# Kernel optimization log

Measured on AMD Instinct MI355X. Metric: run time of the kernel, lower is better.

Reference implementation:

```python
import jax, jax.numpy as jnp
import numpy as np

D_MODEL, N_HEAD, N_BR = 768, 12, 4
DH = D_MODEL // N_HEAD            # 64
H_TOT = N_BR * N_HEAD             # 48
K_RETR = 12
MLP_SCALE = np.pi / np.sqrt(3.0)


def rmsnorm(x):
    eps = jnp.finfo(x.dtype).eps
    return x * jax.lax.rsqrt(jnp.mean(x * x, axis=-1, keepdims=True) + eps)


def setup_inputs() -> dict:
    key = jax.random.key(0)
    ks = jax.random.split(key, 16)
    B, T, C = 2, 1024, D_MODEL
    s = 0.02
    return {
        "A": jax.random.normal(ks[0], (B, T, C), jnp.float32),
        "X": jax.random.normal(ks[1], (B, T, C), jnp.float32),
        "Wq_w": jax.random.normal(ks[2], (4 * C, C), jnp.float32) * s,
        "Wq_b": jax.random.normal(ks[3], (4 * C,), jnp.float32) * s,
        "Wk_w": jax.random.normal(ks[4], (C, C), jnp.float32) * s,
        "Wk_b": jax.random.normal(ks[5], (C,), jnp.float32) * s,
        "wedge_A": jax.random.normal(ks[6], (DH, DH), jnp.float32) * s,
        "wedge_bias": jax.random.normal(ks[7], (H_TOT, DH), jnp.float32) * s,
        "sink_scalars": jax.random.normal(ks[8], (H_TOT, 1, 1), jnp.float32) * s,
        "v_nulls": jax.random.normal(ks[9], (N_BR, C), jnp.float32) * s,
        "fc_w": jax.random.normal(ks[10], (4 * DH, DH), jnp.float32) * s,
        "fc_b": jax.random.normal(ks[11], (4 * DH,), jnp.float32) * s,
        "proj_w": jax.random.normal(ks[12], (DH, 4 * DH), jnp.float32) * s,
        "proj_b": jax.random.normal(ks[13], (DH,), jnp.float32) * s,
        "WO": jax.random.normal(ks[14], (N_BR, C, C), jnp.float32) * s,
        "WO_b": jax.random.normal(ks[15], (N_BR, C), jnp.float32) * s,
    }


def reference(A, X, Wq_w, Wq_b, Wk_w, Wk_b, wedge_A, wedge_bias,
              sink_scalars, v_nulls, fc_w, fc_b, proj_w, proj_b, WO, WO_b):
    B, T, C = A.shape
    K = min(K_RETR, T)
    scale = DH ** -0.5

    # Q / K projections -> (B, H, T, Dh)
    q = (A @ Wq_w.T + Wq_b).reshape(B, T, H_TOT, DH).transpose(0, 2, 1, 3)
    q = rmsnorm(q)
    kb = (X @ Wk_w.T + Wk_b).reshape(B, T, N_HEAD, DH).transpose(0, 2, 1, 3)
    k = jnp.tile(kb, (1, N_BR, 1, 1))          # repeat sub-heads over branches
    k_vanilla = k                               # pre-wedge/pre-rope keys

    # BiasedWedge: x + x @ (skew(A) + diag(id_bias)) per head
    S = (wedge_A - wedge_A.T) + jax.vmap(jnp.diag)(wedge_bias)   # (H, Dh, Dh)
    q = q + jnp.einsum('bhtd,hde->bhte', q, S)
    k = k + jnp.einsum('bhtd,hde->bhte', k, S)

    # RoPE (interleaved halves concatenated)
    inv_freq = 1.0 / (10000.0 ** (jnp.arange(0, DH, 2, dtype=jnp.float32) / DH))
    freqs = jnp.arange(T, dtype=jnp.float32)[:, None] * inv_freq[None, :]  # (T, Dh/2)
    cos, sin = jnp.cos(freqs), jnp.sin(freqs)

    def rope(x):
        x1, x2 = x[..., 0::2], x[..., 1::2]
        return jnp.concatenate([x1 * cos - x2 * sin, x1 * sin + x2 * cos], axis=-1)

    q, k = rope(q), rope(k)

    # full causal attention with sink token
    scores = jnp.einsum('bhtd,bhsd->bhts', q, k) * scale        # (B,H,T,T)
    causal = jnp.triu(jnp.ones((T, T), bool), 1)
    scores = jnp.where(causal, -jnp.inf, scores)
    sinks = jnp.broadcast_to(sink_scalars.reshape(1, H_TOT, 1, 1), (B, H_TOT, T, 1))
    probs = jax.nn.softmax(jnp.concatenate([scores, sinks], axis=-1), axis=-1)
    probs_tok = jnp.where(causal, 0.0, probs[..., :T])
    probs_sink = probs[..., T:]                                  # (B,H,T,1)

    # top-k retrieval + gather of vanilla keys
    w, idx = jax.lax.top_k(probs_tok, K)                         # (B,H,T,K)
    bi = jnp.arange(B)[:, None, None, None]
    hi = jnp.arange(H_TOT)[None, :, None, None]
    k_sel = k_vanilla[bi, hi, idx]                               # (B,H,T,K,Dh)
    # weighted mean marker (sum is permutation-invariant, so sort is elided)
    marker = (jnp.einsum('bhtk,bhtkd->bhtd', w, k_sel) + k_vanilla) / (K + 1)

    # per-token V_net MLP on head_dim
    h = marker @ fc_w.T + fc_b
    h = h * h + 0.75 * h * h * h
    h = rmsnorm(h)
    h = h * jax.nn.sigmoid(MLP_SCALE * h)
    out_tokens = h @ proj_w.T + proj_b                           # (B,H,T,Dh)

    context = out_tokens + probs_sink * v_nulls.reshape(H_TOT, DH)[None, :, None, :]
    context = context.reshape(B, N_BR, N_HEAD, T, DH).transpose(0, 1, 3, 2, 4)
    context = context.reshape(B, N_BR, T, C)

    y = jnp.einsum('bntc,ncd->bntd', context, WO) + WO_b[None, :, None, :]
    return y.mean(axis=1)
```

## Files before the change

kernel.cpp:

```cpp
#include <hip/hip_runtime.h>
#include <math.h>

#define B_   2
#define T_   1024
#define C_   768
#define DH_  64
#define NH_  12
#define HT_  48

typedef short bf16x8 __attribute__((ext_vector_type(8)));
typedef float f32x4 __attribute__((ext_vector_type(4)));

__device__ __forceinline__ float wave_sum(float v) {
#pragma unroll
    for (int off = 32; off; off >>= 1) v += __shfl_xor(v, off, 64);
    return v;
}
__device__ __forceinline__ unsigned short rne_bf16(float f) {
    unsigned u = __float_as_uint(f);
    return (unsigned short)((u + 0x7FFFu + ((u >> 16) & 1u)) >> 16);
}
__device__ __forceinline__ float bf2f(unsigned short u) {
    return __uint_as_float((unsigned)u << 16);
}

#define LOG2E 1.4426950408889634f
#define KBIAS 32.0f

__constant__ int c_tileTab[40] = {15,15,15,15, 14,14,14, 13,13,13, 12,12,12, 11,11,11,
                                  10,10, 9,9, 8,8, 7,7, 6, 5, 4, 3,
                                  14,10,6,2, 13,9,5,1, 12,8,4,0};
__constant__ int c_partTab[40] = { 0, 1, 2, 3,  0, 1, 2,  0, 1, 2,  0, 1, 2,  0, 1, 2,
                                   0, 1, 0,1, 0,1, 0,1, 0, 0, 0, 0,
                                   3, 2,1,0,  3,2,1,0,  3,2,1,0};

__global__ __launch_bounds__(256) void prep_all(
    const float* __restrict__ wA, const float* __restrict__ wb, const float* __restrict__ WOb,
    const float* __restrict__ A, const float* __restrict__ X,
    const float* __restrict__ Wq, const float* __restrict__ Wk,
    const float* __restrict__ fcw, const float* __restrict__ pw, const float* __restrict__ WO,
    float* __restrict__ S, float* __restrict__ rc, float* __restrict__ rs, float* __restrict__ wob,
    unsigned short* __restrict__ Ab, unsigned short* __restrict__ Xb,
    unsigned short* __restrict__ Wqb, unsigned short* __restrict__ Wkb,
    unsigned short* __restrict__ fcb, unsigned short* __restrict__ pwb,
    unsigned short* __restrict__ WOt) {
    __shared__ float tl[32][33];
    const int bid = blockIdx.x;
    if (bid < 2304) {
        const int n = bid / 576, rem = bid % 576;
        const int d0 = (rem / 24) * 32, c0 = (rem % 24) * 32;
        const int tx = threadIdx.x & 31, ty = threadIdx.x >> 5;
#pragma unroll
        for (int p = 0; p < 4; p++)
            tl[ty + p * 8][tx] = WO[(size_t)n * 589824 + (size_t)(c0 + ty + p * 8) * 768 + d0 + tx];
        __syncthreads();
#pragma unroll
        for (int p = 0; p < 4; p++)
            WOt[(size_t)(d0 + ty + p * 8) * 3072 + n * 768 + c0 + tx] = rne_bf16(tl[tx][ty + p * 8]);
    } else if (bid < 8288) {
        int i = (bid - 2304) * 256 + threadIdx.x;
        const float* s; unsigned short* d; int o;
        if (i < 393216)       { s = A;   d = Ab;  o = i; }
        else if (i < 786432)  { s = X;   d = Xb;  o = i - 393216; }
        else if (i < 1376256) { s = Wq;  d = Wqb; o = i - 786432; }
        else if (i < 1523712) { s = Wk;  d = Wkb; o = i - 1376256; }
        else if (i < 1527808) { s = fcw; d = fcb; o = i - 1523712; }
        else if (i < 1531904) { s = pw;  d = pwb; o = i - 1527808; }
        else return;
        float4 v = reinterpret_cast<const float4*>(s)[o];
        ushort4 u;
        u.x = rne_bf16(v.x); u.y = rne_bf16(v.y); u.z = rne_bf16(v.z); u.w = rne_bf16(v.w);
        reinterpret_cast<ushort4*>(d)[o] = u;
    } else {
        int i = (bid - 8288) * 256 + threadIdx.x;
        if (i < HT_ * 64 * 64) {
            int e = i & 63, d = (i >> 6) & 63, h = i >> 12;
            float v = wA[d * 64 + e] - wA[e * 64 + d];
            if (d == e) v += wb[h * 64 + d];
            S[i] = v;
        } else if (i < HT_ * 64 * 64 + T_ * 32) {
            int j = i - HT_ * 64 * 64;
            int t = j >> 5, f = j & 31;
            float invf = (float)(1.0 / pow(10000.0, (double)f / 32.0));
            float fr = (float)t * invf;
            rc[j] = cosf(fr);
            rs[j] = sinf(fr);
        } else if (i < HT_ * 64 * 64 + T_ * 32 + C_) {
            int d = i - (HT_ * 64 * 64 + T_ * 32);
            wob[d] = WOb[d] + WOb[C_ + d] + WOb[2 * C_ + d] + WOb[3 * C_ + d];
        }
    }
}

__global__ __launch_bounds__(256) void gemm_qk(
    const unsigned short* __restrict__ Aq, const unsigned short* __restrict__ Wqw,
    const float* __restrict__ bq, float* __restrict__ Cq,
    const unsigned short* __restrict__ Ak, const unsigned short* __restrict__ Wkw,
    const float* __restrict__ bk, float* __restrict__ Ck,
    unsigned short* __restrict__ kvb) {
    __shared__ unsigned short Asd[128][40];
    __shared__ unsigned short Bsd[128][40];
    int bx = blockIdx.x;
    const bool isK = (bx >= 24);
    const unsigned short *A, *W; const float* bias; float* C; int N;
    if (!isK) { A = Aq; W = Wqw; bias = bq; C = Cq; N = 3072; }
    else { bx -= 24; A = Ak; W = Wkw; bias = bk; C = Ck; N = 768; }
    const int K = 768;
    const int tid = threadIdx.x;
    const int wv = tid >> 6, lane = tid & 63;
    const int m0 = blockIdx.y * 128, n0 = bx * 128;
    const int wr = (wv >> 1) * 64, wc = (wv & 1) * 64;
    const int l15 = lane & 15, l4 = lane >> 4;
    const int srow = tid >> 2, soff = (tid & 3) * 8;
    f32x4 acc[4][4] = {};
    for (int k0 = 0; k0 < K; k0 += 32) {
        uint4 a0 = *reinterpret_cast<const uint4*>(A + (size_t)(m0 + srow) * K + k0 + soff);
        uint4 a1 = *reinterpret_cast<const uint4*>(A + (size_t)(m0 + srow + 64) * K + k0 + soff);
        uint4 b0 = *reinterpret_cast<const uint4*>(W + (size_t)(n0 + srow) * K + k0 + soff);
        uint4 b1 = *reinterpret_cast<const uint4*>(W + (size_t)(n0 + srow + 64) * K + k0 + soff);
        *reinterpret_cast<uint4*>(&Asd[srow][soff])      = a0;
        *reinterpret_cast<uint4*>(&Asd[srow + 64][soff]) = a1;
        *reinterpret_cast<uint4*>(&Bsd[srow][soff])      = b0;
        *reinterpret_cast<uint4*>(&Bsd[srow + 64][soff]) = b1;
        __syncthreads();
        bf16x8 af[4], bfr[4];
#pragma unroll
        for (int i = 0; i < 4; i++)
            af[i] = *reinterpret_cast<const bf16x8*>(&Asd[wr + i * 16 + l15][l4 * 8]);
#pragma unroll
        for (int j = 0; j < 4; j++)
            bfr[j] = *reinterpret_cast<const bf16x8*>(&Bsd[wc + j * 16 + l15][l4 * 8]);
#pragma unroll
        for (int i = 0; i < 4; i++)
#pragma unroll
            for (int j = 0; j < 4; j++)
                acc[i][j] = __builtin_amdgcn_mfma_f32_16x16x32_bf16(af[i], bfr[j], acc[i][j], 0, 0, 0);
        __syncthreads();
    }
#pragma unroll
    for (int i = 0; i < 4; i++)
#pragma unroll
        for (int j = 0; j < 4; j++) {
            int col = n0 + wc + j * 16 + l15;
            float bv = bias[col];
#pragma unroll
            for (int r = 0; r < 4; r++) {
                int row = m0 + wr + i * 16 + l4 * 4 + r;
                float o = acc[i][j][r] + bv;
                C[(size_t)row * N + col] = o;
                if (isK) {
                    int hk2 = col >> 6, d2 = col & 63;
                    int bb = row >> 10, tt = row & 1023;
                    kvb[((((size_t)(bb * 12 + hk2)) << 10) + tt) * 64 + d2] = rne_bf16(o);
                }
            }
        }
}

__global__ __launch_bounds__(256) void gemm_wo_splitk(const unsigned short* __restrict__ A,
                                                      const unsigned short* __restrict__ W,
                                                      float* __restrict__ Cp) {
    __shared__ unsigned short Asd[64][40];
    __shared__ unsigned short Bsd[64][40];
    const int tid = threadIdx.x;
    const int wv = tid >> 6, lane = tid & 63;
    const int m0 = blockIdx.y * 64, n0 = blockIdx.x * 64, z = blockIdx.z;
    const int l15 = lane & 15, l4 = lane >> 4;
    const int srow = tid >> 2, soff = (tid & 3) * 8;
    const int K = 3072;
    float* C = Cp + (size_t)z * 1572864;
    f32x4 acc[4] = {};
    for (int k0 = z * 768; k0 < z * 768 + 768; k0 += 32) {
        uint4 a0 = *reinterpret_cast<const uint4*>(A + (size_t)(m0 + srow) * K + k0 + soff);
        uint4 b0 = *reinterpret_cast<const uint4*>(W + (size_t)(n0 + srow) * K + k0 + soff);
        *reinterpret_cast<uint4*>(&Asd[srow][soff]) = a0;
        *reinterpret_cast<uint4*>(&Bsd[srow][soff]) = b0;
        __syncthreads();
        bf16x8 af = *reinterpret_cast<const bf16x8*>(&Asd[wv * 16 + l15][l4 * 8]);
#pragma unroll
        for (int j = 0; j < 4; j++) {
            bf16x8 bfr = *reinterpret_cast<const bf16x8*>(&Bsd[j * 16 + l15][l4 * 8]);
            acc[j] = __builtin_amdgcn_mfma_f32_16x16x32_bf16(af, bfr, acc[j], 0, 0, 0);
        }
        __syncthreads();
    }
#pragma unroll
    for (int j = 0; j < 4; j++) {
        int col = n0 + j * 16 + l15;
#pragma unroll
        for (int r = 0; r < 4; r++) {
            int row = m0 + wv * 16 + l4 * 4 + r;
            C[(size_t)row * 768 + col] = acc[j][r];
        }
    }
}

__global__ __launch_bounds__(256) void wo_reduce(const float* __restrict__ Cp,
                                                 const float* __restrict__ wob,
                                                 float* __restrict__ out) {
    int i = blockIdx.x * 256 + threadIdx.x;
    const float4* p0 = reinterpret_cast<const float4*>(Cp);
    const float4* p1 = reinterpret_cast<const float4*>(Cp + 1572864);
    const float4* p2 = reinterpret_cast<const float4*>(Cp + 3145728);
    const float4* p3 = reinterpret_cast<const float4*>(Cp + 4718592);
    float4 a = p0[i], b = p1[i], c = p2[i], d = p3[i];
    float4 w = reinterpret_cast<const float4*>(wob)[i % 192];
    float4 o;
    o.x = (a.x + b.x + c.x + d.x + w.x) * 0.25f;
    o.y = (a.y + b.y + c.y + d.y + w.y) * 0.25f;
    o.z = (a.z + b.z + c.z + d.z + w.z) * 0.25f;
    o.w = (a.w + b.w + c.w + d.w + w.w) * 0.25f;
    reinterpret_cast<float4*>(out)[i] = o;
}

__global__ __launch_bounds__(256) void transform_qk(
    const float* __restrict__ qb, const float* __restrict__ kbv, const float* __restrict__ S,
    const float* __restrict__ rc, const float* __restrict__ rs,
    unsigned short* __restrict__ qhi, unsigned short* __restrict__ qlo,
    unsigned short* __restrict__ khi, unsigned short* __restrict__ klo) {
    const int tid = threadIdx.x, wv = tid >> 6, lane = tid & 63;
    const bool isQ = blockIdx.x < 1536;
    const int bidx = isQ ? blockIdx.x : blockIdx.x - 1536;
    const int h = bidx >> 5, blk = bidx & 31;
    const int hk = h % 12;
    __shared__ float Sl[4096];
    __shared__ float sh[4][64];
    const float4* Sg = reinterpret_cast<const float4*>(S + h * 4096);
#pragma unroll
    for (int i = 0; i < 4; i++)
        reinterpret_cast<float4*>(Sl)[tid + 256 * i] = Sg[tid + 256 * i];
    __syncthreads();
    unsigned short* ohi = isQ ? qhi : khi;
    unsigned short* olo = isQ ? qlo : klo;
    for (int it = 0; it < 16; ++it) {
        int r = (blk << 6) + (wv << 4) + it;
        int b = r >> 10, t = r & 1023;
        float v;
        if (isQ) {
            v = qb[((((size_t)(b << 10) + t) * 48 + h) << 6) + lane];
            float ss = wave_sum(v * v);
            v *= 1.f / sqrtf(ss * (1.f / 64.f) + 1.1920928955078125e-07f);
        } else {
            v = kbv[((((size_t)(b << 10) + t) * 12 + hk) << 6) + lane];
        }
        sh[wv][lane] = v;
        float acc = v;
#pragma unroll 8
        for (int d = 0; d < 64; d++) acc = fmaf(sh[wv][d], Sl[(d << 6) + lane], acc);
        sh[wv][lane] = acc;
        int j = lane & 31;
        float x1 = sh[wv][2 * j], x2 = sh[wv][2 * j + 1];
        float ct = rc[t * 32 + j], st = rs[t * 32 + j];
        float o = (lane < 32) ? (x1 * ct - x2 * st) : (x1 * st + x2 * ct);
        if (isQ) o *= 0.125f * LOG2E;
        unsigned short oh = rne_bf16(o);
        unsigned short ol = rne_bf16(o - bf2f(oh));
        size_t oidx = ((((size_t)(b * 48 + h)) << 10) + t) * 64 + lane;
        ohi[oidx] = oh;
        olo[oidx] = ol;
    }
}

#define POPQ(qq)                                                                  \
    {                                                                             \
        bool tk = (qq[0] == hm);                                                  \
        qq[0]=tk?qq[1]:qq[0]; qq[1]=tk?qq[2]:qq[1]; qq[2]=tk?qq[3]:qq[2];         \
        qq[3]=tk?qq[4]:qq[3]; qq[4]=tk?qq[5]:qq[4]; qq[5]=tk?qq[6]:qq[5];         \
        qq[6]=tk?qq[7]:qq[6]; qq[7]=tk?qq[8]:qq[7]; qq[8]=tk?qq[9]:qq[8];         \
        qq[9]=tk?qq[10]:qq[9]; qq[10]=tk?qq[11]:qq[10]; qq[11]=tk?0u:qq[11];      \
    }

#define TOP12INS(pln, pk)                                                         \
    {                                                                             \
        unsigned _p = (pk);                                                       \
        _Pragma("unroll")                                                         \
        for (int jj = 0; jj < 12; jj++) {                                         \
            unsigned mx = pln[jj] > _p ? pln[jj] : _p;                            \
            _p = pln[jj] > _p ? _p : pln[jj];                                     \
            pln[jj] = mx;                                                         \
        }                                                                         \
    }

__global__ __launch_bounds__(64, 3) void attn_scores(
    const unsigned short* __restrict__ qhi, const unsigned short* __restrict__ qlo,
    const unsigned short* __restrict__ khi, const unsigned short* __restrict__ klo,
    float* __restrict__ pZ, unsigned int* __restrict__ pP) {
    const int lane = threadIdx.x;
    const int bid = blockIdx.x;
    const int u = bid / 96, bh = bid % 96;
    const int tile = c_tileTab[u >> 1], part = c_partTab[u >> 1], half = u & 1;
    const int l15 = lane & 15, l4 = lane >> 4;
    const int t0 = (tile << 6) + (half << 5);
    const int c0 = part << 2;
    const int c1 = min(c0 + 4, tile + 1);
    const size_t base = ((size_t)bh) << 16;

    bf16x8 qh8[2][2], ql8[2][2];
#pragma unroll
    for (int ni = 0; ni < 2; ni++)
#pragma unroll
        for (int ks = 0; ks < 2; ks++) {
            size_t off = base + (size_t)(t0 + ni * 16 + l15) * 64 + ks * 32 + l4 * 8;
            qh8[ni][ks] = *reinterpret_cast<const bf16x8*>(qhi + off);
            ql8[ni][ks] = *reinterpret_cast<const bf16x8*>(qlo + off);
        }

    unsigned int pl[2][12];
#pragma unroll
    for (int ni = 0; ni < 2; ni++)
#pragma unroll
        for (int i = 0; i < 12; i++) pl[ni][i] = 0u;
    float Zp[2] = {0.f, 0.f};

    for (int cc = c0; cc < c1; ++cc) {
        f32x4 acc[4][2];
#pragma unroll
        for (int mi = 0; mi < 4; mi++)
#pragma unroll
            for (int ni = 0; ni < 2; ni++)
                acc[mi][ni] = (f32x4){KBIAS, KBIAS, KBIAS, KBIAS};
#pragma unroll
        for (int ks = 0; ks < 2; ks++) {
            bf16x8 kh8[4], kl8[4];
#pragma unroll
            for (int mi = 0; mi < 4; mi++) {
                size_t off = base + (size_t)((cc << 6) + mi * 16 + l15) * 64 + ks * 32 + l4 * 8;
                kh8[mi] = *reinterpret_cast<const bf16x8*>(khi + off);
                kl8[mi] = *reinterpret_cast<const bf16x8*>(klo + off);
            }
#pragma unroll
            for (int mi = 0; mi < 4; mi++)
#pragma unroll
                for (int ni = 0; ni < 2; ni++) {
                    acc[mi][ni] = __builtin_amdgcn_mfma_f32_16x16x32_bf16(kh8[mi], qh8[ni][ks], acc[mi][ni], 0, 0, 0);
                    acc[mi][ni] = __builtin_amdgcn_mfma_f32_16x16x32_bf16(kh8[mi], ql8[ni][ks], acc[mi][ni], 0, 0, 0);
                    acc[mi][ni] = __builtin_amdgcn_mfma_f32_16x16x32_bf16(kl8[mi], qh8[ni][ks], acc[mi][ni], 0, 0, 0);
                }
        }
        if (cc == tile) {
#pragma unroll
            for (int ni = 0; ni < 2; ni++) {
                const int tq = t0 + ni * 16 + l15;
#pragma unroll
                for (int mi = 0; mi < 4; mi++)
#pragma unroll
                    for (int r = 0; r < 4; r++) {
                        int kcol = (cc << 6) + mi * 16 + l4 * 4 + r;
                        float s = acc[mi][ni][r];
                        bool ok = kcol <= tq;
                        float e = exp2f(s);
                        Zp[ni] += ok ? e : 0.f;
                        unsigned pk = (__float_as_uint(s) & 0xFFFFFC00u) | (unsigned)(1023 - kcol);
                        pk = ok ? pk : 0u;
                        TOP12INS(pl[ni], pk);
                    }
            }
        } else {
#pragma unroll
            for (int ni = 0; ni < 2; ni++) {
#pragma unroll
                for (int mi = 0; mi < 4; mi++)
#pragma unroll
                    for (int r = 0; r < 4; r++) {
                        int kcol = (cc << 6) + mi * 16 + l4 * 4 + r;
                        float s = acc[mi][ni][r];
                        Zp[ni] += exp2f(s);
                        unsigned pk = (__float_as_uint(s) & 0xFFFFFC00u) | (unsigned)(1023 - kcol);
                        TOP12INS(pl[ni], pk);
                    }
            }
        }
    }

    __shared__ unsigned int lsh[64][2][12];
    __shared__ float zsh[64][2];
#pragma unroll
    for (int ni = 0; ni < 2; ni++) {
#pragma unroll
        for (int i = 0; i < 12; i++) lsh[lane][ni][i] = pl[ni][i];
        zsh[lane][ni] = Zp[ni];
    }
    __syncthreads();
    if (lane < 32) {
        const int ni = lane >> 4, c = lane & 15;
        unsigned int m0[12], m1[12], m2[12], m3[12];
#pragma unroll
        for (int i = 0; i < 12; i++) {
            m0[i] = lsh[c][ni][i];
            m1[i] = lsh[c + 16][ni][i];
            m2[i] = lsh[c + 32][ni][i];
            m3[i] = lsh[c + 48][ni][i];
        }
        float Z = zsh[c][ni] + zsh[c + 16][ni] + zsh[c + 32][ni] + zsh[c + 48][ni];
        unsigned int out[12];
#pragma unroll
        for (int rd = 0; rd < 12; rd++) {
            unsigned int ha = m0[0] > m1[0] ? m0[0] : m1[0];
            unsigned int hb2 = m2[0] > m3[0] ? m2[0] : m3[0];
            unsigned int hm = ha > hb2 ? ha : hb2;
            POPQ(m0); POPQ(m1); POPQ(m2); POPQ(m3);
            out[rd] = hm;
        }
        const size_t r = (((size_t)bh) << 10) + t0 + lane;
        pZ[r * 4 + part] = Z;
        unsigned int* pp = pP + r * 48 + part * 12;
        *reinterpret_cast<uint4*>(pp + 0) = make_uint4(out[0], out[1], out[2], out[3]);
        *reinterpret_cast<uint4*>(pp + 4) = make_uint4(out[4], out[5], out[6], out[7]);
        *reinterpret_cast<uint4*>(pp + 8) = make_uint4(out[8], out[9], out[10], out[11]);
    }
}

__global__ __launch_bounds__(256, 2) void mlp_fused(
    const unsigned int* __restrict__ pP, const float* __restrict__ pZ,
    const float* __restrict__ sink_s, const unsigned short* __restrict__ kvb,
    const unsigned short* __restrict__ fcw, const float* __restrict__ fcb,
    const unsigned short* __restrict__ pw, const float* __restrict__ pb,
    const float* __restrict__ vn, unsigned short* __restrict__ ctx) {
    const int tid = threadIdx.x, wv = tid >> 6, lane = tid & 63;
    const int l15 = lane & 15, l4 = lane >> 4;
    const int wid = blockIdx.x * 4 + wv;
    const int r0 = wid << 4;
    const int bh = wid >> 6;
    const int h = bh % 48, b = bh / 48, hk = h % 12;
    const int tbase = r0 & 1023;
    const int tile = tbase >> 6;
    const int npart = (tile >> 2) + 1;
    __shared__ __align__(16) char scratch[4][8704];
    __shared__ unsigned int idwi[4][16][12];
    __shared__ float idww[4][16][12];

    const int row = r0 + l15;
    unsigned int qq[12];
    {
        const bool val = l4 < npart;
        uint4 x0 = make_uint4(0,0,0,0), x1 = x0, x2 = x0;
        if (val) {
            const uint4* ip = reinterpret_cast<const uint4*>(pP + (size_t)row * 48 + l4 * 12);
            x0 = ip[0]; x1 = ip[1]; x2 = ip[2];
        }
        qq[0]=x0.x; qq[1]=x0.y; qq[2]=x0.z; qq[3]=x0.w;
        qq[4]=x1.x; qq[5]=x1.y; qq[6]=x1.z; qq[7]=x1.w;
        qq[8]=x2.x; qq[9]=x2.y; qq[10]=x2.z; qq[11]=x2.w;
    }
    float Zl = (l4 < npart) ? pZ[(size_t)row * 4 + l4] : 0.f;
    float Z = Zl;
    Z += __shfl_xor(Z, 16, 64);
    Z += __shfl_xor(Z, 32, 64);
    const float es = exp2f(sink_s[h] * LOG2E + KBIAS);
    const float invZ = 1.f / (Z + es);
    const float psink = es * invZ;

#pragma unroll
    for (int rd = 0; rd < 12; rd++) {
        unsigned int m = qq[0];
        unsigned int o1 = __shfl_xor(m, 16, 64); m = m > o1 ? m : o1;
        unsigned int o2 = __shfl_xor(m, 32, 64); m = m > o2 ? m : o2;
        const unsigned int hm = m;
        POPQ(qq);
        if (l4 == 0) {
            idwi[wv][l15][rd] = 1023u - (hm & 1023u);
            idww[wv][l15][rd] = (hm == 0u) ? 0.f : exp2f(__uint_as_float(hm & 0xFFFFFC00u)) * invZ;
        }
    }
    __syncthreads();

    const unsigned short* kvroot = kvb + (((size_t)(b * 12 + hk)) << 16);
    float acc4[4][4];
#pragma unroll
    for (int i = 0; i < 4; i++)
#pragma unroll
        for (int e = 0; e < 4; e++) acc4[i][e] = 0.f;
#pragma unroll
    for (int rsub = 0; rsub < 4; rsub++) {
        const int grow = rsub * 4 + l4;
#pragma unroll
        for (int rr = 0; rr < 12; rr++) {
            unsigned idx = idwi[wv][grow][rr];
            float w = idww[wv][grow][rr];
            ushort4 kv = *reinterpret_cast<const ushort4*>(kvroot + ((size_t)idx << 6) + l15 * 4);
            acc4[rsub][0] = fmaf(w, bf2f(kv.x), acc4[rsub][0]);
            acc4[rsub][1] = fmaf(w, bf2f(kv.y), acc4[rsub][1]);
            acc4[rsub][2] = fmaf(w, bf2f(kv.z), acc4[rsub][2]);
            acc4[rsub][3] = fmaf(w, bf2f(kv.w), acc4[rsub][3]);
        }
        ushort4 kv = *reinterpret_cast<const ushort4*>(kvroot + ((size_t)(tbase + grow) << 6) + l15 * 4);
        acc4[rsub][0] = (acc4[rsub][0] + bf2f(kv.x)) * (1.f / 13.f);
        acc4[rsub][1] = (acc4[rsub][1] + bf2f(kv.y)) * (1.f / 13.f);
        acc4[rsub][2] = (acc4[rsub][2] + bf2f(kv.z)) * (1.f / 13.f);
        acc4[rsub][3] = (acc4[rsub][3] + bf2f(kv.w)) * (1.f / 13.f);
    }

    float* mkls = reinterpret_cast<float*>(scratch[wv]);
#pragma unroll
    for (int rsub = 0; rsub < 4; rsub++)
        *reinterpret_cast<float4*>(&mkls[(rsub * 4 + l4) * 68 + l15 * 4]) =
            make_float4(acc4[rsub][0], acc4[rsub][1], acc4[rsub][2], acc4[rsub][3]);
    __syncthreads();
    bf16x8 amk[2];
#pragma unroll
    for (int ks = 0; ks < 2; ks++) {
        float4 f0 = *reinterpret_cast<const float4*>(&mkls[l15 * 68 + ks * 32 + l4 * 8]);
        float4 f1 = *reinterpret_cast<const float4*>(&mkls[l15 * 68 + ks * 32 + l4 * 8 + 4]);
        amk[ks][0] = (short)rne_bf16(f0.x); amk[ks][1] = (short)rne_bf16(f0.y);
        amk[ks][2] = (short)rne_bf16(f0.z); amk[ks][3] = (short)rne_bf16(f0.w);
        amk[ks][4] = (short)rne_bf16(f1.x); amk[ks][5] = (short)rne_bf16(f1.y);
        amk[ks][6] = (short)rne_bf16(f1.z); amk[ks][7] = (short)rne_bf16(f1.w);
    }
    __syncthreads();

    f32x4 hacc[16] = {};
#pragma unroll
    for (int ks = 0; ks < 2; ks++)
#pragma unroll
        for (int j = 0; j < 16; j++) {
            bf16x8 bw = *reinterpret_cast<const bf16x8*>(fcw + (j * 16 + l15) * 64 + ks * 32 + l4 * 8);
            hacc[j] = __builtin_amdgcn_mfma_f32_16x16x32_bf16(amk[ks], bw, hacc[j], 0, 0, 0);
        }

    float ss[4] = {0.f, 0.f, 0.f, 0.f};
#pragma unroll
    for (int j = 0; j < 16; j++) {
        float bv = fcb[j * 16 + l15];
#pragma unroll
        for (int r = 0; r < 4; r++) {
            float x = hacc[j][r] + bv;
            float y = x * x + 0.75f * x * x * x;
            hacc[j][r] = y;
            ss[r] = fmaf(y, y, ss[r]);
        }
    }
#pragma unroll
    for (int m = 1; m < 16; m <<= 1)
#pragma unroll
        for (int r = 0; r < 4; r++) ss[r] += __shfl_xor(ss[r], m, 64);
    float rinv[4];
#pragma unroll
    for (int r = 0; r < 4; r++)
        rinv[r] = 1.f / sqrtf(ss[r] * (1.f / 256.f) + 1.1920928955078125e-07f);
    unsigned short (*hsd)[272] = reinterpret_cast<unsigned short (*)[272]>(scratch[wv]);
#pragma unroll
    for (int j = 0; j < 16; j++)
#pragma unroll
        for (int r = 0; r < 4; r++) {
            float z = hacc[j][r] * rinv[r];
            float g = z / (1.f + exp2f(-2.616571036720458f * z));
            hsd[l4 * 4 + r][j * 16 + l15] = rne_bf16(g);
        }
    __syncthreads();

    f32x4 oacc[4] = {};
#pragma unroll
    for (int ks = 0; ks < 8; ks++) {
        bf16x8 ah = *reinterpret_cast<const bf16x8*>(&hsd[l15][ks * 32 + l4 * 8]);
#pragma unroll
        for (int j = 0; j < 4; j++) {
            bf16x8 bw = *reinterpret_cast<const bf16x8*>(pw + (j * 16 + l15) * 256 + ks * 32 + l4 * 8);
            oacc[j] = __builtin_amdgcn_mfma_f32_16x16x32_bf16(ah, bw, oacc[j], 0, 0, 0);
        }
    }
#pragma unroll
    for (int j = 0; j < 4; j++) {
        int d = j * 16 + l15;
        float pbv = pb[d];
        float vnv = vn[h * 64 + d];
#pragma unroll
        for (int r = 0; r < 4; r++) {
            int rloc = l4 * 4 + r;
            int t = tbase + rloc;
            float p = __shfl(psink, rloc, 64);
            float o = oacc[j][r] + pbv + p * vnv;
            ctx[((((size_t)(b << 10) + t) * 48 + h) << 6) + d] = rne_bf16(o);
        }
    }
}

extern "C" void kernel_launch(void* const* d_in, const int* in_sizes, int n_in,
                              void* d_out, int out_size, void* d_ws, size_t ws_size,
                              hipStream_t stream) {
    (void)in_sizes; (void)n_in; (void)out_size; (void)ws_size;
    const float* A       = (const float*)d_in[0];
    const float* X       = (const float*)d_in[1];
    const float* Wq_w    = (const float*)d_in[2];
    const float* Wq_b    = (const float*)d_in[3];
    const float* Wk_w    = (const float*)d_in[4];
    const float* Wk_b    = (const float*)d_in[5];
    const float* wedge_A = (const float*)d_in[6];
    const float* wedge_b = (const float*)d_in[7];
    const float* sink    = (const float*)d_in[8];
    const float* v_nulls = (const float*)d_in[9];
    const float* fc_w    = (const float*)d_in[10];
    const float* fc_b    = (const float*)d_in[11];
    const float* proj_w  = (const float*)d_in[12];
    const float* proj_b  = (const float*)d_in[13];
    const float* WO      = (const float*)d_in[14];
    const float* WO_b    = (const float*)d_in[15];
    float* out = (float*)d_out;
    float* ws  = (float*)d_ws;

    float*          qbuf   = ws;
    unsigned short* ctx_bf = (unsigned short*)ws;
    float*          kbbuf  = ws + 6291456;
    unsigned short* q_hi   = (unsigned short*)(ws + 7864320);
    float*          wop    = ws + 7864320;
    unsigned short* q_lo   = (unsigned short*)(ws + 11010048);
    unsigned short* kf_hi  = (unsigned short*)(ws + 14155776);
    unsigned short* kf_lo  = (unsigned short*)(ws + 17301504);
    unsigned short* A_bf   = (unsigned short*)(ws + 20447232);
    unsigned short* X_bf   = (unsigned short*)(ws + 21233664);
    unsigned short* Wq_bf  = (unsigned short*)(ws + 22020096);
    unsigned short* Wk_bf  = (unsigned short*)(ws + 23199744);
    float*          Sbuf   = ws + 23494656;
    float*          rcbuf  = ws + 23691264;
    float*          rsbuf  = ws + 23724032;
    float*          pZ     = ws + 20447232;
    unsigned int*   pP     = (unsigned int*)(ws + 20840448);
    float*          wob    = ws + 25559040;
    unsigned short* fcw_bf = (unsigned short*)(ws + 25560064);
    unsigned short* pw_bf  = (unsigned short*)(ws + 25568256);
    unsigned short* WOt_bf = (unsigned short*)(ws + 25576448);
    unsigned short* kvb    = (unsigned short*)(ws + 26756096);

    prep_all<<<9187, 256, 0, stream>>>(wedge_A, wedge_b, WO_b,
                                       A, X, Wq_w, Wk_w, fc_w, proj_w, WO,
                                       Sbuf, rcbuf, rsbuf, wob,
                                       A_bf, X_bf, Wq_bf, Wk_bf, fcw_bf, pw_bf, WOt_bf);
    gemm_qk<<<dim3(30, 16), 256, 0, stream>>>(A_bf, Wq_bf, Wq_b, qbuf,
                                              X_bf, Wk_bf, Wk_b, kbbuf, kvb);
    transform_qk<<<3072, 256, 0, stream>>>(qbuf, kbbuf, Sbuf, rcbuf, rsbuf,
                                           q_hi, q_lo, kf_hi, kf_lo);
    attn_scores<<<7680, 64, 0, stream>>>(q_hi, q_lo, kf_hi, kf_lo, pZ, pP);
    mlp_fused<<<1536, 256, 0, stream>>>(pP, pZ, sink, kvb,
                                        fcw_bf, fc_b, pw_bf, proj_b, v_nulls, ctx_bf);
    gemm_wo_splitk<<<dim3(12, 32, 4), 256, 0, stream>>>(ctx_bf, WOt_bf, wop);
    wo_reduce<<<1536, 256, 0, stream>>>(wop, wob, out);
}
```

Measured before the change: 291.2 us.

## Compute wedge transform with split-bf16 MFMA instead of scalar FMA loop

```diff
diff --git a/kernel.cpp b/kernel.cpp
--- a/kernel.cpp
+++ b/kernel.cpp
@@ -39,7 +39,8 @@
     const float* __restrict__ A, const float* __restrict__ X,
     const float* __restrict__ Wq, const float* __restrict__ Wk,
     const float* __restrict__ fcw, const float* __restrict__ pw, const float* __restrict__ WO,
-    float* __restrict__ S, float* __restrict__ rc, float* __restrict__ rs, float* __restrict__ wob,
+    unsigned short* __restrict__ sthi, unsigned short* __restrict__ stlo,
+    float* __restrict__ rc, float* __restrict__ rs, float* __restrict__ wob,
     unsigned short* __restrict__ Ab, unsigned short* __restrict__ Xb,
     unsigned short* __restrict__ Wqb, unsigned short* __restrict__ Wkb,
     unsigned short* __restrict__ fcb, unsigned short* __restrict__ pwb,
@@ -74,10 +75,14 @@
     } else {
         int i = (bid - 8288) * 256 + threadIdx.x;
         if (i < HT_ * 64 * 64) {
-            int e = i & 63, d = (i >> 6) & 63, h = i >> 12;
+            int d = i & 63, c = (i >> 6) & 63, h2 = i >> 12;
+            int j = c >> 4, i15 = c & 15;
+            int e = (j & 1) + 2 * (((j >> 1) << 4) + i15);
             float v = wA[d * 64 + e] - wA[e * 64 + d];
-            if (d == e) v += wb[h * 64 + d];
-            S[i] = v;
+            if (d == e) v += 1.f + wb[h2 * 64 + e];
+            unsigned short hi = rne_bf16(v);
+            sthi[i] = hi;
+            stlo[i] = rne_bf16(v - bf2f(hi));
         } else if (i < HT_ * 64 * 64 + T_ * 32) {
             int j = i - HT_ * 64 * 64;
             int t = j >> 5, f = j & 31;
@@ -213,51 +218,91 @@
     reinterpret_cast<float4*>(out)[i] = o;
 }
 
-__global__ __launch_bounds__(256) void transform_qk(
-    const float* __restrict__ qb, const float* __restrict__ kbv, const float* __restrict__ S,
+__global__ __launch_bounds__(256) void transform_qk2(
+    const float* __restrict__ qb, const float* __restrict__ kbv,
+    const unsigned short* __restrict__ sthi, const unsigned short* __restrict__ stlo,
     const float* __restrict__ rc, const float* __restrict__ rs,
     unsigned short* __restrict__ qhi, unsigned short* __restrict__ qlo,
     unsigned short* __restrict__ khi, unsigned short* __restrict__ klo) {
     const int tid = threadIdx.x, wv = tid >> 6, lane = tid & 63;
-    const bool isQ = blockIdx.x < 1536;
-    const int bidx = isQ ? blockIdx.x : blockIdx.x - 1536;
-    const int h = bidx >> 5, blk = bidx & 31;
+    const int l15 = lane & 15, l4 = lane >> 4;
+    const int wid = blockIdx.x * 4 + wv;
+    const bool isQ = wid < 6144;
+    const int widl = isQ ? wid : wid - 6144;
+    const int h = widl >> 7;
+    const int rbase = (widl & 127) << 4;
     const int hk = h % 12;
-    __shared__ float Sl[4096];
-    __shared__ float sh[4][64];
-    const float4* Sg = reinterpret_cast<const float4*>(S + h * 4096);
-#pragma unroll
-    for (int i = 0; i < 4; i++)
-        reinterpret_cast<float4*>(Sl)[tid + 256 * i] = Sg[tid + 256 * i];
-    __syncthreads();
+
+    bf16x8 ah[2], al[2];
+    {
+        int rg = rbase + l15;
+        int b = rg >> 10, t = rg & 1023;
+        const float* src = isQ
+            ? qb + ((((size_t)(b << 10) + t) * 48 + h) << 6)
+            : kbv + ((((size_t)(b << 10) + t) * 12 + hk) << 6);
+        float4 f0 = *reinterpret_cast<const float4*>(src + l4 * 8);
+        float4 f1 = *reinterpret_cast<const float4*>(src + l4 * 8 + 4);
+        float4 f2 = *reinterpret_cast<const float4*>(src + 32 + l4 * 8);
+        float4 f3 = *reinterpret_cast<const float4*>(src + 32 + l4 * 8 + 4);
+        if (isQ) {
+            float ss = f0.x*f0.x + f0.y*f0.y + f0.z*f0.z + f0.w*f0.w
+                     + f1.x*f1.x + f1.y*f1.y + f1.z*f1.z + f1.w*f1.w
+                     + f2.x*f2.x + f2.y*f2.y + f2.z*f2.z + f2.w*f2.w
+                     + f3.x*f3.x + f3.y*f3.y + f3.z*f3.z + f3.w*f3.w;
+            ss += __shfl_xor(ss, 16, 64);
+            ss += __shfl_xor(ss, 32, 64);
+            float sc = 1.f / sqrtf(ss * (1.f / 64.f) + 1.1920928955078125e-07f);
+            f0.x *= sc; f0.y *= sc; f0.z *= sc; f0.w *= sc;
+            f1.x *= sc; f1.y *= sc; f1.z *= sc; f1.w *= sc;
+            f2.x *= sc; f2.y *= sc; f2.z *= sc; f2.w *= sc;
+            f3.x *= sc; f3.y *= sc; f3.z *= sc; f3.w *= sc;
+        }
+        float v0[8] = {f0.x, f0.y, f0.z, f0.w, f1.x, f1.y, f1.z, f1.w};
+        float v1[8] = {f2.x, f2.y, f2.z, f2.w, f3.x, f3.y, f3.z, f3.w};
+#pragma unroll
+        for (int e = 0; e < 8; e++) {
+            unsigned short h0 = rne_bf16(v0[e]);
+            ah[0][e] = (short)h0; al[0][e] = (short)rne_bf16(v0[e] - bf2f(h0));
+            unsigned short h1 = rne_bf16(v1[e]);
+            ah[1][e] = (short)h1; al[1][e] = (short)rne_bf16(v1[e] - bf2f(h1));
+        }
+    }
+
+    const unsigned short* sh_ = sthi + (h << 12);
+    const unsigned short* sl_ = stlo + (h << 12);
+    f32x4 acc[4] = {};
+#pragma unroll
+    for (int ks = 0; ks < 2; ks++)
+#pragma unroll
+        for (int j = 0; j < 4; j++) {
+            bf16x8 bh = *reinterpret_cast<const bf16x8*>(sh_ + (j * 16 + l15) * 64 + ks * 32 + l4 * 8);
+            bf16x8 bl = *reinterpret_cast<const bf16x8*>(sl_ + (j * 16 + l15) * 64 + ks * 32 + l4 * 8);
+            acc[j] = __builtin_amdgcn_mfma_f32_16x16x32_bf16(ah[ks], bh, acc[j], 0, 0, 0);
+            acc[j] = __builtin_amdgcn_mfma_f32_16x16x32_bf16(al[ks], bh, acc[j], 0, 0, 0);
+            acc[j] = __builtin_amdgcn_mfma_f32_16x16x32_bf16(ah[ks], bl, acc[j], 0, 0, 0);
+        }
+
     unsigned short* ohi = isQ ? qhi : khi;
     unsigned short* olo = isQ ? qlo : klo;
-    for (int it = 0; it < 16; ++it) {
-        int r = (blk << 6) + (wv << 4) + it;
-        int b = r >> 10, t = r & 1023;
-        float v;
-        if (isQ) {
-            v = qb[((((size_t)(b << 10) + t) * 48 + h) << 6) + lane];
-            float ss = wave_sum(v * v);
-            v *= 1.f / sqrtf(ss * (1.f / 64.f) + 1.1920928955078125e-07f);
-        } else {
-            v = kbv[((((size_t)(b << 10) + t) * 12 + hk) << 6) + lane];
-        }
-        sh[wv][lane] = v;
-        float acc = v;
-#pragma unroll 8
-        for (int d = 0; d < 64; d++) acc = fmaf(sh[wv][d], Sl[(d << 6) + lane], acc);
-        sh[wv][lane] = acc;
-        int j = lane & 31;
-        float x1 = sh[wv][2 * j], x2 = sh[wv][2 * j + 1];
-        float ct = rc[t * 32 + j], st = rs[t * 32 + j];
-        float o = (lane < 32) ? (x1 * ct - x2 * st) : (x1 * st + x2 * ct);
-        if (isQ) o *= 0.125f * LOG2E;
-        unsigned short oh = rne_bf16(o);
-        unsigned short ol = rne_bf16(o - bf2f(oh));
-        size_t oidx = ((((size_t)(b * 48 + h)) << 10) + t) * 64 + lane;
-        ohi[oidx] = oh;
-        olo[oidx] = ol;
+    const float qscl = 0.125f * LOG2E;
+#pragma unroll
+    for (int r = 0; r < 4; r++) {
+        int rg = rbase + l4 * 4 + r;
+        int b = rg >> 10, t = rg & 1023;
+        float c0 = rc[t * 32 + l15],      s0 = rs[t * 32 + l15];
+        float c1 = rc[t * 32 + 16 + l15], s1 = rs[t * 32 + 16 + l15];
+        float o0 = acc[0][r] * c0 - acc[1][r] * s0;
+        float o2 = acc[0][r] * s0 + acc[1][r] * c0;
+        float o1 = acc[2][r] * c1 - acc[3][r] * s1;
+        float o3 = acc[2][r] * s1 + acc[3][r] * c1;
+        if (isQ) { o0 *= qscl; o1 *= qscl; o2 *= qscl; o3 *= qscl; }
+        size_t obase = ((((size_t)(b * 48 + h)) << 10) + t) * 64;
+        unsigned short h0 = rne_bf16(o0), h1 = rne_bf16(o1);
+        unsigned short h2 = rne_bf16(o2), h3 = rne_bf16(o3);
+        ohi[obase + l15]      = h0;  olo[obase + l15]      = rne_bf16(o0 - bf2f(h0));
+        ohi[obase + 16 + l15] = h1;  olo[obase + 16 + l15] = rne_bf16(o1 - bf2f(h1));
+        ohi[obase + 32 + l15] = h2;  olo[obase + 32 + l15] = rne_bf16(o2 - bf2f(h2));
+        ohi[obase + 48 + l15] = h3;  olo[obase + 48 + l15] = rne_bf16(o3 - bf2f(h3));
     }
 }
 
@@ -609,7 +654,8 @@
     unsigned short* X_bf   = (unsigned short*)(ws + 21233664);
     unsigned short* Wq_bf  = (unsigned short*)(ws + 22020096);
     unsigned short* Wk_bf  = (unsigned short*)(ws + 23199744);
-    float*          Sbuf   = ws + 23494656;
+    unsigned short* Sthi   = (unsigned short*)(ws + 23494656);
+    unsigned short* Stlo   = (unsigned short*)(ws + 23592960);
     float*          rcbuf  = ws + 23691264;
     float*          rsbuf  = ws + 23724032;
     float*          pZ     = ws + 20447232;
@@ -622,12 +668,12 @@
 
     prep_all<<<9187, 256, 0, stream>>>(wedge_A, wedge_b, WO_b,
                                        A, X, Wq_w, Wk_w, fc_w, proj_w, WO,
-                                       Sbuf, rcbuf, rsbuf, wob,
+                                       Sthi, Stlo, rcbuf, rsbuf, wob,
                                        A_bf, X_bf, Wq_bf, Wk_bf, fcw_bf, pw_bf, WOt_bf);
     gemm_qk<<<dim3(30, 16), 256, 0, stream>>>(A_bf, Wq_bf, Wq_b, qbuf,
                                               X_bf, Wk_bf, Wk_b, kbbuf, kvb);
-    transform_qk<<<3072, 256, 0, stream>>>(qbuf, kbbuf, Sbuf, rcbuf, rsbuf,
-                                           q_hi, q_lo, kf_hi, kf_lo);
+    transform_qk2<<<3072, 256, 0, stream>>>(qbuf, kbbuf, Sthi, Stlo, rcbuf, rsbuf,
+                                            q_hi, q_lo, kf_hi, kf_lo);
     attn_scores<<<7680, 64, 0, stream>>>(q_hi, q_lo, kf_hi, kf_lo, pZ, pP);
     mlp_fused<<<1536, 256, 0, stream>>>(pP, pZ, sink, kvb,
                                         fcw_bf, fc_b, pw_bf, proj_b, v_nulls, ctx_bf);
```

New measurement: 246.2 us. -15.4%, faster.
